# Performance work log

Measured on AMD Instinct MI355X. Metric: run time of the kernel, lower is better.

Reference implementation:

```python
import jax, jax.numpy as jnp
import numpy as np

# Each of the 16 binary logic gates, relaxed to real values, is a multilinear
# function: gate(a,b) = c0 + c1*a + c2*b + c3*a*b. Rows follow the standard
# difflogic ordering: FALSE, AND, a&~b, a, ~a&b, b, XOR, OR, NOR, XNOR,
# ~b, a|~b, ~a, ~a|b, NAND, TRUE.
GATE_COEF = jnp.array([
    [0.0,  0.0,  0.0,  0.0],   # 0:  false
    [0.0,  0.0,  0.0,  1.0],   # 1:  a AND b
    [0.0,  1.0,  0.0, -1.0],   # 2:  a AND NOT b
    [0.0,  1.0,  0.0,  0.0],   # 3:  a
    [0.0,  0.0,  1.0, -1.0],   # 4:  NOT a AND b
    [0.0,  0.0,  1.0,  0.0],   # 5:  b
    [0.0,  1.0,  1.0, -2.0],   # 6:  a XOR b
    [0.0,  1.0,  1.0, -1.0],   # 7:  a OR b
    [1.0, -1.0, -1.0,  1.0],   # 8:  NOR
    [1.0, -1.0, -1.0,  2.0],   # 9:  XNOR
    [1.0,  0.0, -1.0,  0.0],   # 10: NOT b
    [1.0,  0.0, -1.0,  1.0],   # 11: a OR NOT b
    [1.0, -1.0,  0.0,  0.0],   # 12: NOT a
    [1.0, -1.0,  0.0,  1.0],   # 13: NOT a OR b
    [1.0,  0.0,  0.0, -1.0],   # 14: NAND
    [1.0,  0.0,  0.0,  0.0],   # 15: true
], dtype=jnp.float32)

B, IN_DIM, HIDDEN, N_LAYERS, OUT_DIM, TAU = 4096, 1024, 8192, 6, 8, 10.0
NPO = HIDDEN // OUT_DIM  # neurons_per_output


def logic_layer(h, w, ia, ib):
    # h: [B, in_dim]; w: [H, 16]; ia, ib: [H] int indices into in_dim.
    # Softmax-weighted blend of 16 gates == multilinear form with blended coefs.
    p = jax.nn.softmax(w, axis=-1)          # [H, 16]
    c = p @ GATE_COEF                       # [H, 4]
    a = h[:, ia]                            # [B, H] gather
    b = h[:, ib]                            # [B, H] gather
    return c[:, 0] + c[:, 1] * a + c[:, 2] * b + c[:, 3] * (a * b)


def setup_inputs() -> dict:
    key = jax.random.key(0)
    ks = jax.random.split(key, 8)
    return {
        "x": jax.random.uniform(ks[0], (B, IN_DIM), dtype=jnp.float32),
        "logic_w": jax.random.normal(ks[1], (N_LAYERS, HIDDEN, 16), dtype=jnp.float32),
        "scaler_w": jax.random.normal(ks[2], (OUT_DIM, OUT_DIM), dtype=jnp.float32) * 0.1,
        "scaler_b": jax.random.normal(ks[3], (OUT_DIM,), dtype=jnp.float32) * 0.1,
        "idx0_a": jax.random.randint(ks[4], (HIDDEN,), 0, IN_DIM, dtype=jnp.int32),
        "idx0_b": jax.random.randint(ks[5], (HIDDEN,), 0, IN_DIM, dtype=jnp.int32),
        "idx_a": jax.random.randint(ks[6], (N_LAYERS - 1, HIDDEN), 0, HIDDEN, dtype=jnp.int32),
        "idx_b": jax.random.randint(ks[7], (N_LAYERS - 1, HIDDEN), 0, HIDDEN, dtype=jnp.int32),
    }


def reference(x, logic_w, scaler_w, scaler_b, idx0_a, idx0_b, idx_a, idx_b):
    h = (x.reshape(x.shape[0], -1) > 0.5).astype(jnp.float32)   # binarize
    h = logic_layer(h, logic_w[0], idx0_a, idx0_b)               # [B, HIDDEN]
    for i in range(N_LAYERS - 1):
        h = logic_layer(h, logic_w[i + 1], idx_a[i], idx_b[i])
    h = h.reshape(h.shape[0], OUT_DIM, NPO)                      # [B, O, NPO]
    values = jnp.sum(h, axis=2) / TAU                            # [B, O]
    q_values = values @ scaler_w.T + scaler_b                    # nn.Linear
    return q_values
```

## Files before the change

### kernel.cpp

```cpp
#include <hip/hip_runtime.h>
#include <hip/hip_fp16.h>

constexpr int BATCH    = 4096;
constexpr int IN_DIM   = 1024;
constexpr int HIDDEN   = 8192;
constexpr int N_LAYERS = 6;
constexpr int OUT_DIM  = 8;
constexpr float INV_TAU = 0.1f;

constexpr int TB   = 16;
constexpr int NTH  = 1024;
constexpr int NPT  = HIDDEN / NTH;
constexpr int NWAVES = NTH / 64;

typedef float v2f __attribute__((ext_vector_type(2)));

__device__ __forceinline__ __half2 u2h(unsigned int u) {
    union { unsigned int u; __half2 h; } v; v.u = u; return v.h;
}
__device__ __forceinline__ unsigned int h2u(__half2 h) {
    union { unsigned int u; __half2 h; } v; v.h = h; return v.u;
}
__device__ __forceinline__ uint2 pack4h(float4 v) {
    __half2 lo = __float22half2_rn(make_float2(v.x, v.y));
    __half2 hi = __float22half2_rn(make_float2(v.z, v.w));
    uint2 r; r.x = h2u(lo); r.y = h2u(hi); return r;
}

__global__ void prep_kernel(const float* __restrict__ logic_w,
                            const int* __restrict__ idx0_a,
                            const int* __restrict__ idx0_b,
                            const int* __restrict__ idx_a,
                            const int* __restrict__ idx_b,
                            uint2* __restrict__ coefp,
                            unsigned int* __restrict__ idxp, int n)
{
    int id = blockIdx.x * blockDim.x + threadIdx.x;
    if (id >= n) return;
    const int l = id / HIDDEN;
    const int j = id - l * HIDDEN;

    int ia, ib;
    if (l == 0) { ia = idx0_a[j]; ib = idx0_b[j]; }
    else        { ia = idx_a[(size_t)(l - 1) * HIDDEN + j];
                  ib = idx_b[(size_t)(l - 1) * HIDDEN + j]; }
    idxp[id] = (unsigned int)ia | ((unsigned int)ib << 16);

    const float4* w4 = (const float4*)(logic_w + (size_t)id * 16);
    float4 wa = w4[0], wb = w4[1], wc = w4[2], wd = w4[3];
    float wv[16] = {wa.x, wa.y, wa.z, wa.w, wb.x, wb.y, wb.z, wb.w,
                    wc.x, wc.y, wc.z, wc.w, wd.x, wd.y, wd.z, wd.w};
    float m = wv[0];
#pragma unroll
    for (int i = 1; i < 16; ++i) m = fmaxf(m, wv[i]);
    float e[16];
    float s = 0.f;
#pragma unroll
    for (int i = 0; i < 16; ++i) { e[i] = expf(wv[i] - m); s += e[i]; }
    float inv = 1.f / s;
    const float G0[16] = {0,0,0,0,0,0,0,0, 1,1,1,1,1,1,1,1};
    const float G1[16] = {0,0,1,1,0,0,1,1, -1,-1,0,0,-1,-1,0,0};
    const float G2[16] = {0,0,0,0,1,1,1,1, -1,-1,-1,-1,0,0,0,0};
    const float G3[16] = {0,1,-1,0,-1,0,-2,-1, 1,2,0,1,0,1,-1,0};
    float c0 = 0.f, c1 = 0.f, c2 = 0.f, c3 = 0.f;
#pragma unroll
    for (int i = 0; i < 16; ++i) {
        float p = e[i] * inv;
        c0 = fmaf(p, G0[i], c0);
        c1 = fmaf(p, G1[i], c1);
        c2 = fmaf(p, G2[i], c2);
        c3 = fmaf(p, G3[i], c3);
    }
    coefp[id] = pack4h(make_float4(c0, c1, c2, c3));
}

__device__ __forceinline__ unsigned int gate4d(unsigned int a8, unsigned int b8,
                                               float c0, float c1, float c2, float c3)
{
    v2f alo = __builtin_amdgcn_cvt_pk_f32_fp8((int)a8, false);
    v2f ahi = __builtin_amdgcn_cvt_pk_f32_fp8((int)a8, true);
    v2f blo = __builtin_amdgcn_cvt_pk_f32_fp8((int)b8, false);
    v2f bhi = __builtin_amdgcn_cvt_pk_f32_fp8((int)b8, true);
    float r0 = fmaf(blo.x, fmaf(c3, alo.x, c2), fmaf(c1, alo.x, c0));
    float r1 = fmaf(blo.y, fmaf(c3, alo.y, c2), fmaf(c1, alo.y, c0));
    float r2 = fmaf(bhi.x, fmaf(c3, ahi.x, c2), fmaf(c1, ahi.x, c0));
    float r3 = fmaf(bhi.y, fmaf(c3, ahi.y, c2), fmaf(c1, ahi.y, c0));
    int w = __builtin_amdgcn_cvt_pk_fp8_f32(r0, r1, 0, false);
    w     = __builtin_amdgcn_cvt_pk_fp8_f32(r2, r3, w, true);
    return (unsigned int)w;
}

__device__ __forceinline__ void gate4d_acc(unsigned int a8, unsigned int b8,
                                           float c0, float c1, float c2, float c3,
                                           float* s)
{
    v2f alo = __builtin_amdgcn_cvt_pk_f32_fp8((int)a8, false);
    v2f ahi = __builtin_amdgcn_cvt_pk_f32_fp8((int)a8, true);
    v2f blo = __builtin_amdgcn_cvt_pk_f32_fp8((int)b8, false);
    v2f bhi = __builtin_amdgcn_cvt_pk_f32_fp8((int)b8, true);
    s[0] += fmaf(blo.x, fmaf(c3, alo.x, c2), fmaf(c1, alo.x, c0));
    s[1] += fmaf(blo.y, fmaf(c3, alo.y, c2), fmaf(c1, alo.y, c0));
    s[2] += fmaf(bhi.x, fmaf(c3, ahi.x, c2), fmaf(c1, ahi.x, c0));
    s[3] += fmaf(bhi.y, fmaf(c3, ahi.y, c2), fmaf(c1, ahi.y, c0));
}

__device__ __forceinline__ uint4 gate16(uint4 a, uint4 b, uint2 c) {
    __half2 cp01 = u2h(c.x), cp23 = u2h(c.y);
    float c0 = __low2float(cp01), c1 = __high2float(cp01);
    float c2 = __low2float(cp23), c3 = __high2float(cp23);
    uint4 r;
    r.x = gate4d(a.x, b.x, c0, c1, c2, c3);
    r.y = gate4d(a.y, b.y, c0, c1, c2, c3);
    r.z = gate4d(a.z, b.z, c0, c1, c2, c3);
    r.w = gate4d(a.w, b.w, c0, c1, c2, c3);
    return r;
}

__device__ __forceinline__ uint4 pack16(const float* f) {
    uint4 r;
    unsigned int* rd = (unsigned int*)&r;
#pragma unroll
    for (int d = 0; d < 4; ++d) {
        int w = __builtin_amdgcn_cvt_pk_fp8_f32(f[4 * d + 0], f[4 * d + 1], 0, false);
        w     = __builtin_amdgcn_cvt_pk_fp8_f32(f[4 * d + 2], f[4 * d + 3], w, true);
        rd[d] = (unsigned int)w;
    }
    return r;
}

__global__ __launch_bounds__(NTH)
__attribute__((amdgpu_waves_per_eu(4, 4)))
void net_kernel(
    const float*  __restrict__ x,
    const uint2*  __restrict__ coefp,
    const unsigned int* __restrict__ idxp,
    const float*  __restrict__ scaler_w, const float* __restrict__ scaler_b,
    float* __restrict__ out)
{
    __shared__ uint4 h[HIDDEN];
    __shared__ uint4 hx[IN_DIM];
    __shared__ float warr[NWAVES][TB];
    __shared__ float vals[TB][OUT_DIM];

    const int tid = threadIdx.x;
    const int b0  = blockIdx.x * TB;
    const int g   = tid >> 7;
    const int t0  = tid & 127;
    const int jb  = g * 1024 + t0;

    {
        float v[TB];
#pragma unroll
        for (int r = 0; r < TB; ++r)
            v[r] = (x[(size_t)(b0 + r) * IN_DIM + tid] > 0.5f) ? 1.f : 0.f;
        hx[tid] = pack16(v);
    }

    unsigned int ij[NPT], ijn[NPT];
    uint4 acc[NPT];

#pragma unroll
    for (int k = 0; k < NPT; ++k) ij[k] = idxp[jb + (k << 7)];

    __syncthreads();

#pragma unroll
    for (int k = 0; k < NPT; ++k) ijn[k] = idxp[HIDDEN + jb + (k << 7)];
#pragma unroll
    for (int k = 0; k < NPT; ++k) {
        unsigned int pr = ij[k];
        acc[k] = gate16(hx[pr & 0xffffu], hx[pr >> 16], coefp[jb + (k << 7)]);
    }
#pragma unroll
    for (int k = 0; k < NPT; ++k) h[jb + (k << 7)] = acc[k];
    __syncthreads();

    for (int l = 1; l < N_LAYERS - 1; ++l) {
#pragma unroll
        for (int k = 0; k < NPT; ++k) ij[k] = ijn[k];
#pragma unroll
        for (int k = 0; k < NPT; ++k)
            ijn[k] = idxp[(size_t)(l + 1) * HIDDEN + jb + (k << 7)];
        const uint2* cp = coefp + (size_t)l * HIDDEN;
#pragma unroll
        for (int k = 0; k < NPT; ++k) {
            unsigned int pr = ij[k];
            acc[k] = gate16(h[pr & 0xffffu], h[pr >> 16], cp[jb + (k << 7)]);
        }
        __syncthreads();
#pragma unroll
        for (int k = 0; k < NPT; ++k) h[jb + (k << 7)] = acc[k];
        __syncthreads();
    }

    float s[TB];
#pragma unroll
    for (int r = 0; r < TB; ++r) s[r] = 0.f;
    {
        const uint2* cp = coefp + (size_t)(N_LAYERS - 1) * HIDDEN;
#pragma unroll
        for (int k = 0; k < NPT; ++k) {
            unsigned int pr = ijn[k];
            uint4 a = h[pr & 0xffffu], b = h[pr >> 16];
            uint2 c = cp[jb + (k << 7)];
            __half2 cp01 = u2h(c.x), cp23 = u2h(c.y);
            float c0 = __low2float(cp01), c1 = __high2float(cp01);
            float c2 = __low2float(cp23), c3 = __high2float(cp23);
            gate4d_acc(a.x, b.x, c0, c1, c2, c3, s + 0);
            gate4d_acc(a.y, b.y, c0, c1, c2, c3, s + 4);
            gate4d_acc(a.z, b.z, c0, c1, c2, c3, s + 8);
            gate4d_acc(a.w, b.w, c0, c1, c2, c3, s + 12);
        }
    }

#pragma unroll
    for (int off = 32; off > 0; off >>= 1) {
#pragma unroll
        for (int r = 0; r < TB; ++r) s[r] += __shfl_down(s[r], off);
    }
    if ((tid & 63) == 0) {
        const int wv = tid >> 6;
#pragma unroll
        for (int r = 0; r < TB; ++r) warr[wv][r] = s[r];
    }
    __syncthreads();
    if (tid < TB * OUT_DIM) {
        int r = tid >> 3;
        int k = tid & 7;
        vals[r][k] = (warr[2 * k][r] + warr[2 * k + 1][r]) * INV_TAU;
    }
    __syncthreads();
    if (tid < TB * OUT_DIM) {
        int r = tid >> 3;
        int o = tid & 7;
        float q = scaler_b[o];
#pragma unroll
        for (int k = 0; k < OUT_DIM; ++k)
            q = fmaf(vals[r][k], scaler_w[o * OUT_DIM + k], q);
        out[(size_t)(b0 + r) * OUT_DIM + o] = q;
    }
}

extern "C" void kernel_launch(void* const* d_in, const int* in_sizes, int n_in,
                              void* d_out, int out_size, void* d_ws, size_t ws_size,
                              hipStream_t stream)
{
    const float* x        = (const float*)d_in[0];
    const float* logic_w  = (const float*)d_in[1];
    const float* scaler_w = (const float*)d_in[2];
    const float* scaler_b = (const float*)d_in[3];
    const int*   idx0_a   = (const int*)d_in[4];
    const int*   idx0_b   = (const int*)d_in[5];
    const int*   idx_a    = (const int*)d_in[6];
    const int*   idx_b    = (const int*)d_in[7];
    float* out = (float*)d_out;

    const int n = N_LAYERS * HIDDEN;
    uint2*        coefp = (uint2*)d_ws;
    unsigned int* idxp  = (unsigned int*)((char*)d_ws + (size_t)n * sizeof(uint2));

    prep_kernel<<<(n + 255) / 256, 256, 0, stream>>>(logic_w, idx0_a, idx0_b,
                                                     idx_a, idx_b, coefp, idxp, n);
    net_kernel<<<BATCH / TB, NTH, 0, stream>>>(x, coefp, idxp,
                                               scaler_w, scaler_b, out);
}
```

Before: 131.6 us.

## Halve batch tile to 8 rows and double-buffer LDS activations

Each block now processes 8 batch rows instead of 16, storing activations as 8 fp8 values (uint2) per neuron. With the smaller per-neuron footprint, two activation buffers fit in shared memory, so each layer reads one buffer and writes the other and needs only one barrier per layer instead of two. The forced 4-waves-per-EU attribute is removed. This doubles the grid and halves the work per gather, so index and coefficient loads are amortised over fewer rows.

Result: faster. 119.6 us (-9.1%).

```diff
diff --git a/kernel.cpp b/kernel.cpp
--- a/kernel.cpp
+++ b/kernel.cpp
@@ -8,7 +8,7 @@
 constexpr int OUT_DIM  = 8;
 constexpr float INV_TAU = 0.1f;
 
-constexpr int TB   = 16;
+constexpr int TB   = 8;
 constexpr int NTH  = 1024;
 constexpr int NPT  = HIDDEN / NTH;
 constexpr int NWAVES = NTH / 64;
@@ -104,41 +104,25 @@
     s[3] += fmaf(bhi.y, fmaf(c3, ahi.y, c2), fmaf(c1, ahi.y, c0));
 }
 
-__device__ __forceinline__ uint4 gate16(uint4 a, uint4 b, uint2 c) {
+__device__ __forceinline__ uint2 gate8d(uint2 a, uint2 b, uint2 c) {
     __half2 cp01 = u2h(c.x), cp23 = u2h(c.y);
     float c0 = __low2float(cp01), c1 = __high2float(cp01);
     float c2 = __low2float(cp23), c3 = __high2float(cp23);
-    uint4 r;
+    uint2 r;
     r.x = gate4d(a.x, b.x, c0, c1, c2, c3);
     r.y = gate4d(a.y, b.y, c0, c1, c2, c3);
-    r.z = gate4d(a.z, b.z, c0, c1, c2, c3);
-    r.w = gate4d(a.w, b.w, c0, c1, c2, c3);
     return r;
 }
 
-__device__ __forceinline__ uint4 pack16(const float* f) {
-    uint4 r;
-    unsigned int* rd = (unsigned int*)&r;
-#pragma unroll
-    for (int d = 0; d < 4; ++d) {
-        int w = __builtin_amdgcn_cvt_pk_fp8_f32(f[4 * d + 0], f[4 * d + 1], 0, false);
-        w     = __builtin_amdgcn_cvt_pk_fp8_f32(f[4 * d + 2], f[4 * d + 3], w, true);
-        rd[d] = (unsigned int)w;
-    }
-    return r;
-}
-
-__global__ __launch_bounds__(NTH)
-__attribute__((amdgpu_waves_per_eu(4, 4)))
-void net_kernel(
+__global__ __launch_bounds__(NTH) void net_kernel(
     const float*  __restrict__ x,
     const uint2*  __restrict__ coefp,
     const unsigned int* __restrict__ idxp,
     const float*  __restrict__ scaler_w, const float* __restrict__ scaler_b,
     float* __restrict__ out)
 {
-    __shared__ uint4 h[HIDDEN];
-    __shared__ uint4 hx[IN_DIM];
+    __shared__ uint2 hbuf[2][HIDDEN];
+    __shared__ uint2 hx[IN_DIM];
     __shared__ float warr[NWAVES][TB];
     __shared__ float vals[TB][OUT_DIM];
 
@@ -153,11 +137,17 @@
 #pragma unroll
         for (int r = 0; r < TB; ++r)
             v[r] = (x[(size_t)(b0 + r) * IN_DIM + tid] > 0.5f) ? 1.f : 0.f;
-        hx[tid] = pack16(v);
+        uint2 p;
+        int w = __builtin_amdgcn_cvt_pk_fp8_f32(v[0], v[1], 0, false);
+        w     = __builtin_amdgcn_cvt_pk_fp8_f32(v[2], v[3], w, true);
+        p.x = (unsigned int)w;
+        w = __builtin_amdgcn_cvt_pk_fp8_f32(v[4], v[5], 0, false);
+        w = __builtin_amdgcn_cvt_pk_fp8_f32(v[6], v[7], w, true);
+        p.y = (unsigned int)w;
+        hx[tid] = p;
     }
 
     unsigned int ij[NPT], ijn[NPT];
-    uint4 acc[NPT];
 
 #pragma unroll
     for (int k = 0; k < NPT; ++k) ij[k] = idxp[jb + (k << 7)];
@@ -169,13 +159,13 @@
 #pragma unroll
     for (int k = 0; k < NPT; ++k) {
         unsigned int pr = ij[k];
-        acc[k] = gate16(hx[pr & 0xffffu], hx[pr >> 16], coefp[jb + (k << 7)]);
-    }
-#pragma unroll
-    for (int k = 0; k < NPT; ++k) h[jb + (k << 7)] = acc[k];
+        hbuf[0][jb + (k << 7)] =
+            gate8d(hx[pr & 0xffffu], hx[pr >> 16], coefp[jb + (k << 7)]);
+    }
     __syncthreads();
 
     for (int l = 1; l < N_LAYERS - 1; ++l) {
+        const int rb = (l + 1) & 1, wb = l & 1;
 #pragma unroll
         for (int k = 0; k < NPT; ++k) ij[k] = ijn[k];
 #pragma unroll
@@ -185,11 +175,9 @@
 #pragma unroll
         for (int k = 0; k < NPT; ++k) {
             unsigned int pr = ij[k];
-            acc[k] = gate16(h[pr & 0xffffu], h[pr >> 16], cp[jb + (k << 7)]);
+            hbuf[wb][jb + (k << 7)] =
+                gate8d(hbuf[rb][pr & 0xffffu], hbuf[rb][pr >> 16], cp[jb + (k << 7)]);
         }
-        __syncthreads();
-#pragma unroll
-        for (int k = 0; k < NPT; ++k) h[jb + (k << 7)] = acc[k];
         __syncthreads();
     }
 
@@ -201,15 +189,13 @@
 #pragma unroll
         for (int k = 0; k < NPT; ++k) {
             unsigned int pr = ijn[k];
-            uint4 a = h[pr & 0xffffu], b = h[pr >> 16];
+            uint2 a = hbuf[0][pr & 0xffffu], b = hbuf[0][pr >> 16];
             uint2 c = cp[jb + (k << 7)];
             __half2 cp01 = u2h(c.x), cp23 = u2h(c.y);
             float c0 = __low2float(cp01), c1 = __high2float(cp01);
             float c2 = __low2float(cp23), c3 = __high2float(cp23);
             gate4d_acc(a.x, b.x, c0, c1, c2, c3, s + 0);
             gate4d_acc(a.y, b.y, c0, c1, c2, c3, s + 4);
-            gate4d_acc(a.z, b.z, c0, c1, c2, c3, s + 8);
-            gate4d_acc(a.w, b.w, c0, c1, c2, c3, s + 12);
         }
     }
 
```
